# Performance work log

Measured on AMD Instinct MI355X. Metric: run time of the kernel, lower is better.

Reference implementation:

```python
import jax, jax.numpy as jnp
import numpy as np

D_MODEL = 768
CTX_DIM = 1024
N_HEAD = 12
N_QUERIES = 256
DIM_HEAD = D_MODEL // N_HEAD  # 64
INNER = DIM_HEAD * N_HEAD     # 768
EPS = 1e-5


def layernorm(x, w, b):
    mu = jnp.mean(x, axis=-1, keepdims=True)
    var = jnp.mean((x - mu) ** 2, axis=-1, keepdims=True)
    return (x - mu) * jax.lax.rsqrt(var + EPS) * w + b


def setup_inputs() -> dict:
    key = jax.random.key(0)
    ks = jax.random.split(key, 9)
    x = jax.random.normal(ks[0], (8, 4096, CTX_DIM), dtype=jnp.float32)
    query = jax.random.normal(ks[1], (N_QUERIES, D_MODEL), dtype=jnp.float32)
    # Linear weights stored [in, out] (y = x @ W)
    Wq = jax.random.normal(ks[2], (D_MODEL, INNER), dtype=jnp.float32) * 0.02
    Wkv = jax.random.normal(ks[3], (CTX_DIM, 2 * INNER), dtype=jnp.float32) * 0.02
    Wout = jax.random.normal(ks[4], (INNER, D_MODEL), dtype=jnp.float32) * 0.02
    ln_q_w = jnp.ones((D_MODEL,), jnp.float32)
    ln_q_b = jnp.zeros((D_MODEL,), jnp.float32)
    ln_k_w = jnp.ones((CTX_DIM,), jnp.float32)
    ln_k_b = jnp.zeros((CTX_DIM,), jnp.float32)
    return {"x": x, "query": query, "ln_q_w": ln_q_w, "ln_q_b": ln_q_b,
            "ln_k_w": ln_k_w, "ln_k_b": ln_k_b, "Wq": Wq, "Wkv": Wkv, "Wout": Wout}


def reference(x, query, ln_q_w, ln_q_b, ln_k_w, ln_k_b, Wq, Wkv, Wout):
    b = x.shape[0]
    h, dh = N_HEAD, DIM_HEAD
    scale = dh ** -0.5
    xk = x[:, None]  # b 1 n d  (m = 1)
    m, n = xk.shape[1], xk.shape[2]
    q = jnp.broadcast_to(query, (b, m) + query.shape)  # b m nq d
    xk = layernorm(xk, ln_k_w, ln_k_b)
    q = layernorm(q, ln_q_w, ln_q_b)
    q = q @ Wq                          # b m nq inner
    kv = xk @ Wkv                       # b m n 2*inner
    k, v = jnp.split(kv, 2, axis=-1)
    def split_heads(t):
        bb, tt, nn, _ = t.shape
        return t.reshape(bb, tt, nn, h, dh).transpose(0, 3, 1, 2, 4)  # b h t n dh
    q, k, v = split_heads(q), split_heads(k), split_heads(v)
    sim = jnp.einsum('bhtid,bhtjd->bhtij', q * scale, k)
    attn = jax.nn.softmax(sim, axis=-1)
    out = jnp.einsum('bhtij,bhtjd->bhtid', attn, v)  # b h t nq dh
    out = out.transpose(0, 2, 3, 1, 4).reshape(b, m, N_QUERIES, INNER)
    return (out @ Wout).squeeze(axis=1)  # b nq d_model
```

## Files before the change

### kernel.cpp

```cpp
#include <hip/hip_runtime.h>
#include <hip/hip_bf16.h>
#include <math.h>

#define B_    8
#define T_    4096
#define CD    1024
#define DM    768
#define NH    12
#define DH    64
#define NQ    256
#define INNER 768
#define NKV   1536
#define MKV   (B_*T_)
#define EPS   1e-5f
#define SCALE 0.125f

typedef __attribute__((ext_vector_type(8))) short short8;
typedef __attribute__((ext_vector_type(4))) float f32x4;

__device__ __forceinline__ unsigned short f2bf(float f) {
  union { __hip_bfloat16 h; unsigned short u; } cv;
  cv.h = __float2bfloat16(f);
  return cv.u;
}

__global__ __launch_bounds__(256) void tbw_kernel(
    const float* __restrict__ s0, unsigned short* __restrict__ d0,
    const float* __restrict__ s1, unsigned short* __restrict__ d1,
    const float* __restrict__ s2, unsigned short* __restrict__ d2) {
  int z = blockIdx.z;
  const float* src; unsigned short* dst; int SR, SC;
  if (z == 0)      { src = s0; dst = d0; SR = CD;    SC = NKV; }
  else if (z == 1) { src = s1; dst = d1; SR = DM;    SC = INNER; }
  else             { src = s2; dst = d2; SR = INNER; SC = DM; }
  int k0 = blockIdx.x * 32, n0 = blockIdx.y * 32;
  if (k0 >= SR || n0 >= SC) return;
  __shared__ float tile[32][33];
  int tid = threadIdx.x;
  int r = tid >> 3, c4 = (tid & 7) * 4;
  float4 v = *reinterpret_cast<const float4*>(&src[(size_t)(k0 + r) * SC + n0 + c4]);
  tile[r][c4 + 0] = v.x; tile[r][c4 + 1] = v.y; tile[r][c4 + 2] = v.z; tile[r][c4 + 3] = v.w;
  __syncthreads();
  ushort4 o4;
  o4.x = f2bf(tile[c4 + 0][r]);
  o4.y = f2bf(tile[c4 + 1][r]);
  o4.z = f2bf(tile[c4 + 2][r]);
  o4.w = f2bf(tile[c4 + 3][r]);
  *reinterpret_cast<ushort4*>(&dst[(size_t)(n0 + r) * SR + k0 + c4]) = o4;
}

__global__ __launch_bounds__(256) void qln_kernel(
    const float* __restrict__ query, const float* __restrict__ lnw,
    const float* __restrict__ lnb, unsigned short* __restrict__ qn) {
  int row = blockIdx.x, tid = threadIdx.x;
  __shared__ float rbuf[256];
  const float* qr = query + (size_t)row * DM;
  float v0 = qr[tid], v1 = qr[tid + 256], v2 = qr[tid + 512];
  rbuf[tid] = v0 + v1 + v2;
  __syncthreads();
  for (int o = 128; o > 0; o >>= 1) { if (tid < o) rbuf[tid] += rbuf[tid + o]; __syncthreads(); }
  float mean = rbuf[0] * (1.f / 768.f);
  __syncthreads();
  float d0 = v0 - mean, d1 = v1 - mean, d2 = v2 - mean;
  rbuf[tid] = d0 * d0 + d1 * d1 + d2 * d2;
  __syncthreads();
  for (int o = 128; o > 0; o >>= 1) { if (tid < o) rbuf[tid] += rbuf[tid + o]; __syncthreads(); }
  float var = rbuf[0] * (1.f / 768.f);
  float rs = rsqrtf(var + EPS);
  unsigned short* dst = qn + (size_t)row * DM;
  dst[tid]       = f2bf(d0 * rs * lnw[tid]       + lnb[tid]);
  dst[tid + 256] = f2bf(d1 * rs * lnw[tid + 256] + lnb[tid + 256]);
  dst[tid + 512] = f2bf(d2 * rs * lnw[tid + 512] + lnb[tid + 512]);
}

__global__ __launch_bounds__(256) void xnorm_kernel(
    const float* __restrict__ x, const float* __restrict__ lnw,
    const float* __restrict__ lnb, unsigned short* __restrict__ xn) {
  int row = blockIdx.x, tid = threadIdx.x;
  float4 v = reinterpret_cast<const float4*>(x + (size_t)row * CD)[tid];
  float s  = v.x + v.y + v.z + v.w;
  float ss = v.x * v.x + v.y * v.y + v.z * v.z + v.w * v.w;
  #pragma unroll
  for (int o = 32; o > 0; o >>= 1) { s += __shfl_down(s, o); ss += __shfl_down(ss, o); }
  __shared__ float sm[8];
  int wid = tid >> 6, lane = tid & 63;
  if (lane == 0) { sm[wid] = s; sm[4 + wid] = ss; }
  __syncthreads();
  float S  = sm[0] + sm[1] + sm[2] + sm[3];
  float SS = sm[4] + sm[5] + sm[6] + sm[7];
  float m  = S * (1.f / 1024.f);
  float var = SS * (1.f / 1024.f) - m * m;
  float rs = rsqrtf(fmaxf(var, 0.f) + EPS);
  float4 wv = reinterpret_cast<const float4*>(lnw)[tid];
  float4 bv = reinterpret_cast<const float4*>(lnb)[tid];
  ushort4 o4;
  o4.x = f2bf((v.x - m) * rs * wv.x + bv.x);
  o4.y = f2bf((v.y - m) * rs * wv.y + bv.y);
  o4.z = f2bf((v.z - m) * rs * wv.z + bv.z);
  o4.w = f2bf((v.w - m) * rs * wv.w + bv.w);
  reinterpret_cast<ushort4*>(xn + (size_t)row * CD)[tid] = o4;
}

template <int MODE>
__global__ __launch_bounds__(256) void gemm128_kernel(
    const unsigned short* __restrict__ A, const unsigned short* __restrict__ Bt,
    void* __restrict__ Cout, int N, int K, int nN, float scale, int swz) {
  __shared__ __attribute__((aligned(16))) unsigned short As[128 * 64];
  __shared__ __attribute__((aligned(16))) unsigned short Bs[128 * 64];
  int tid = threadIdx.x;
  int w = tid >> 6, lane = tid & 63;
  int bid = blockIdx.x;
  int sw = swz ? ((bid & 7) * ((int)gridDim.x >> 3) + (bid >> 3)) : bid;
  int mt = sw / nN, nt = sw % nN;
  int m0 = mt * 128, n0 = nt * 128;

  int srow[4], skoff[4];
  #pragma unroll
  for (int i = 0; i < 4; ++i) {
    int L = w * 4096 + i * 1024 + lane * 16;
    int row = L >> 7;
    int slot = (L >> 4) & 7;
    srow[i] = row;
    skoff[i] = ((slot ^ (row & 7)) << 3);
  }

  f32x4 acc[4][4];
  #pragma unroll
  for (int m = 0; m < 4; ++m)
    #pragma unroll
    for (int n = 0; n < 4; ++n) acc[m][n] = (f32x4){0.f, 0.f, 0.f, 0.f};

  int wr = w >> 1, wc = w & 1;
  int l15 = lane & 15, l4 = lane >> 4;

  for (int t = 0; t < K / 64; ++t) {
    int k0 = t * 64;
    #pragma unroll
    for (int i = 0; i < 4; ++i) {
      __builtin_amdgcn_global_load_lds(
          (const __attribute__((address_space(1))) void*)(A + (size_t)(m0 + srow[i]) * K + k0 + skoff[i]),
          (__attribute__((address_space(3))) void*)(As + w * 2048 + i * 512 + lane * 8),
          16, 0, 0);
    }
    #pragma unroll
    for (int i = 0; i < 4; ++i) {
      __builtin_amdgcn_global_load_lds(
          (const __attribute__((address_space(1))) void*)(Bt + (size_t)(n0 + srow[i]) * K + k0 + skoff[i]),
          (__attribute__((address_space(3))) void*)(Bs + w * 2048 + i * 512 + lane * 8),
          16, 0, 0);
    }
    __syncthreads();
    #pragma unroll
    for (int kh = 0; kh < 2; ++kh) {
      short8 af[4], bf[4];
      #pragma unroll
      for (int m = 0; m < 4; ++m) {
        int row = wr * 64 + m * 16 + l15;
        int byte = row * 128 + (((l4 + 4 * kh) ^ (row & 7)) << 4);
        af[m] = *reinterpret_cast<const short8*>(reinterpret_cast<const char*>(As) + byte);
      }
      #pragma unroll
      for (int n = 0; n < 4; ++n) {
        int row = wc * 64 + n * 16 + l15;
        int byte = row * 128 + (((l4 + 4 * kh) ^ (row & 7)) << 4);
        bf[n] = *reinterpret_cast<const short8*>(reinterpret_cast<const char*>(Bs) + byte);
      }
      #pragma unroll
      for (int m = 0; m < 4; ++m)
        #pragma unroll
        for (int n = 0; n < 4; ++n)
          acc[m][n] = __builtin_amdgcn_mfma_f32_16x16x32_bf16(af[m], bf[n], acc[m][n], 0, 0, 0);
    }
    __syncthreads();
  }

  #pragma unroll
  for (int m = 0; m < 4; ++m) {
    int grow = m0 + wr * 64 + m * 16 + l4 * 4;
    #pragma unroll
    for (int n = 0; n < 4; ++n) {
      int gcol = n0 + wc * 64 + n * 16 + l15;
      #pragma unroll
      for (int r = 0; r < 4; ++r) {
        if (MODE == 0)
          ((unsigned short*)Cout)[(size_t)(grow + r) * N + gcol] = f2bf(acc[m][n][r] * scale);
        else
          ((float*)Cout)[(size_t)(grow + r) * N + gcol] = acc[m][n][r];
      }
    }
  }
}

#define KBM 256
#define KBN 256
#define KBK 64
__global__ __launch_bounds__(512, 2) void kv_split_kernel(
    const unsigned short* __restrict__ xn, const unsigned short* __restrict__ wkvT,
    unsigned short* __restrict__ kvbK, unsigned short* __restrict__ vT) {
  __shared__ __attribute__((aligned(16))) unsigned short As[2][KBM * KBK];
  __shared__ __attribute__((aligned(16))) unsigned short Bs[2][KBN * KBK];
  int tid = threadIdx.x;
  int w = tid >> 6, lane = tid & 63;
  int wm = w >> 2, wn = w & 3;
  int l15 = lane & 15, l4 = lane >> 4;

  int bid = blockIdx.x;
  int sw = (bid & 7) * 96 + (bid >> 3);
  int mt = sw / (NKV / KBN), nt = sw % (NKV / KBN);
  int m0 = mt * KBM, n0 = nt * KBN;

  int srow[4], koff[4];
  #pragma unroll
  for (int i = 0; i < 4; ++i) {
    int r = i * 64 + (tid >> 3);
    srow[i] = r;
    koff[i] = (((tid & 7) ^ (r & 7)) << 3);
  }

  f32x4 acc[8][4];
  #pragma unroll
  for (int m = 0; m < 8; ++m)
    #pragma unroll
    for (int n = 0; n < 4; ++n) acc[m][n] = (f32x4){0.f, 0.f, 0.f, 0.f};

  #pragma unroll
  for (int i = 0; i < 4; ++i) {
    __builtin_amdgcn_global_load_lds(
        (const __attribute__((address_space(1))) void*)(xn + (size_t)(m0 + srow[i]) * CD + koff[i]),
        (__attribute__((address_space(3))) void*)(&As[0][0] + i * 4096 + tid * 8), 16, 0, 0);
    __builtin_amdgcn_global_load_lds(
        (const __attribute__((address_space(1))) void*)(wkvT + (size_t)(n0 + srow[i]) * CD + koff[i]),
        (__attribute__((address_space(3))) void*)(&Bs[0][0] + i * 4096 + tid * 8), 16, 0, 0);
  }
  __syncthreads();

  for (int t = 0; t < CD / KBK; ++t) {
    int cur = t & 1;
    if (t + 1 < CD / KBK) {
      int k0 = (t + 1) * KBK;
      #pragma unroll
      for (int i = 0; i < 4; ++i) {
        __builtin_amdgcn_global_load_lds(
            (const __attribute__((address_space(1))) void*)(xn + (size_t)(m0 + srow[i]) * CD + k0 + koff[i]),
            (__attribute__((address_space(3))) void*)(&As[cur ^ 1][0] + i * 4096 + tid * 8), 16, 0, 0);
        __builtin_amdgcn_global_load_lds(
            (const __attribute__((address_space(1))) void*)(wkvT + (size_t)(n0 + srow[i]) * CD + k0 + koff[i]),
            (__attribute__((address_space(3))) void*)(&Bs[cur ^ 1][0] + i * 4096 + tid * 8), 16, 0, 0);
      }
    }
    const char* Ab = reinterpret_cast<const char*>(&As[cur][0]);
    const char* Bb = reinterpret_cast<const char*>(&Bs[cur][0]);
    #pragma unroll
    for (int kh = 0; kh < 2; ++kh) {
      short8 bf[4];
      #pragma unroll
      for (int n = 0; n < 4; ++n) {
        int row = wn * 64 + n * 16 + l15;
        int byt = row * 128 + (((kh * 4 + l4) ^ (row & 7)) << 4);
        bf[n] = *reinterpret_cast<const short8*>(Bb + byt);
      }
      #pragma unroll
      for (int m = 0; m < 8; ++m) {
        int row = wm * 128 + m * 16 + l15;
        int byt = row * 128 + (((kh * 4 + l4) ^ (row & 7)) << 4);
        short8 af = *reinterpret_cast<const short8*>(Ab + byt);
        #pragma unroll
        for (int n = 0; n < 4; ++n)
          acc[m][n] = __builtin_amdgcn_mfma_f32_16x16x32_bf16(af, bf[n], acc[m][n], 0, 0, 0);
      }
    }
    __syncthreads();
  }

  if (nt < 3) {
    #pragma unroll
    for (int m = 0; m < 8; ++m) {
      int grow = m0 + wm * 128 + m * 16 + l4 * 4;
      #pragma unroll
      for (int n = 0; n < 4; ++n) {
        int gcol = nt * 256 + wn * 64 + n * 16 + l15;
        #pragma unroll
        for (int r = 0; r < 4; ++r)
          kvbK[(size_t)(grow + r) * INNER + gcol] = f2bf(acc[m][n][r]);
      }
    }
  } else {
    int b = m0 >> 12;
    int h = (nt - 3) * 4 + wn;
    #pragma unroll
    for (int m = 0; m < 8; ++m) {
      int j = (m0 & 4095) + wm * 128 + m * 16 + l4 * 4;
      #pragma unroll
      for (int n = 0; n < 4; ++n) {
        int d = n * 16 + l15;
        ushort4 o4;
        o4.x = f2bf(acc[m][n][0]); o4.y = f2bf(acc[m][n][1]);
        o4.z = f2bf(acc[m][n][2]); o4.w = f2bf(acc[m][n][3]);
        *reinterpret_cast<ushort4*>(&vT[((size_t)(b * NH + h) * DH + d) * T_ + j]) = o4;
      }
    }
  }
}

__global__ __launch_bounds__(256) void attn_mfma_kernel(
    const unsigned short* __restrict__ qpb, const unsigned short* __restrict__ kvbK,
    const unsigned short* __restrict__ vT,
    float* __restrict__ pO, float* __restrict__ pM, float* __restrict__ pL) {
  int bh = blockIdx.x, kc = blockIdx.y, qt = blockIdx.z;
  int b = bh / NH, h = bh % NH;
  __shared__ __attribute__((aligned(16))) unsigned short Ks[2][4096];
  __shared__ __attribute__((aligned(16))) unsigned short Vs[2][4096];
  __shared__ __attribute__((aligned(16))) unsigned short Ps[4][1024];
  int tid = threadIdx.x;
  int w = tid >> 6, lane = tid & 63;
  int l15 = lane & 15, l4 = lane >> 4;

  short8 qf[2];
  {
    const unsigned short* qb = qpb + (size_t)(qt * 64 + w * 16 + l15) * INNER + h * DH;
    qf[0] = *reinterpret_cast<const short8*>(qb + l4 * 8);
    qf[1] = *reinterpret_cast<const short8*>(qb + 32 + l4 * 8);
  }

  int srow0 = w * 16 + (lane >> 3);
  int srow1 = srow0 + 8;
  int koff0 = (((lane & 7) ^ (srow0 & 7)) << 3);
  int koff1 = (((lane & 7) ^ (srow1 & 7)) << 3);

  const size_t kbase = ((size_t)b * T_) * INNER + h * DH;
  const size_t vbase = ((size_t)bh * DH) * T_;

  auto stageKV = [&](int kt, int d) {
    int j0 = kc * 2048 + kt * 64;
    __builtin_amdgcn_global_load_lds(
        (const __attribute__((address_space(1))) void*)(kvbK + kbase + (size_t)(j0 + srow0) * INNER + koff0),
        (__attribute__((address_space(3))) void*)(&Ks[d][0] + w * 1024 + lane * 8), 16, 0, 0);
    __builtin_amdgcn_global_load_lds(
        (const __attribute__((address_space(1))) void*)(kvbK + kbase + (size_t)(j0 + srow1) * INNER + koff1),
        (__attribute__((address_space(3))) void*)(&Ks[d][0] + w * 1024 + 512 + lane * 8), 16, 0, 0);
    __builtin_amdgcn_global_load_lds(
        (const __attribute__((address_space(1))) void*)(vT + vbase + (size_t)srow0 * T_ + j0 + koff0),
        (__attribute__((address_space(3))) void*)(&Vs[d][0] + w * 1024 + lane * 8), 16, 0, 0);
    __builtin_amdgcn_global_load_lds(
        (const __attribute__((address_space(1))) void*)(vT + vbase + (size_t)srow1 * T_ + j0 + koff1),
        (__attribute__((address_space(3))) void*)(&Vs[d][0] + w * 1024 + 512 + lane * 8), 16, 0, 0);
  };

  f32x4 o[4];
  #pragma unroll
  for (int i = 0; i < 4; ++i) o[i] = (f32x4){0.f, 0.f, 0.f, 0.f};
  float m_run = -1e30f, l_run = 0.f;

  stageKV(0, 0);

  for (int kt = 0; kt < 32; ++kt) {
    int cur = kt & 1;
    if (kt + 1 < 32) {
      stageKV(kt + 1, cur ^ 1);
      asm volatile("s_waitcnt vmcnt(4)" ::: "memory");
    } else {
      asm volatile("s_waitcnt vmcnt(0)" ::: "memory");
    }
    __builtin_amdgcn_s_barrier();
    __builtin_amdgcn_sched_barrier(0);

    const char* Kb = reinterpret_cast<const char*>(&Ks[cur][0]);
    const char* Vb = reinterpret_cast<const char*>(&Vs[cur][0]);

    f32x4 st[4];
    __builtin_amdgcn_s_setprio(1);
    #pragma unroll
    for (int sub = 0; sub < 4; ++sub) {
      st[sub] = (f32x4){0.f, 0.f, 0.f, 0.f};
      #pragma unroll
      for (int hf = 0; hf < 2; ++hf) {
        int row = sub * 16 + l15;
        int byt = row * 128 + (((l4 + 4 * hf) ^ (row & 7)) << 4);
        short8 kf = *reinterpret_cast<const short8*>(Kb + byt);
        st[sub] = __builtin_amdgcn_mfma_f32_16x16x32_bf16(kf, qf[hf], st[sub], 0, 0, 0);
      }
    }
    __builtin_amdgcn_s_setprio(0);

    float tmax = -1e30f;
    #pragma unroll
    for (int sub = 0; sub < 4; ++sub)
      #pragma unroll
      for (int r = 0; r < 4; ++r) tmax = fmaxf(tmax, st[sub][r]);
    tmax = fmaxf(tmax, __shfl_xor(tmax, 16));
    tmax = fmaxf(tmax, __shfl_xor(tmax, 32));

    if (__ballot(tmax > m_run + 8.f)) {
      float m_new = fmaxf(m_run, tmax);
      float alpha = __expf(m_run - m_new);
      float ao[4];
      #pragma unroll
      for (int r = 0; r < 4; ++r) ao[r] = __shfl(alpha, (l4 << 2) | r);
      #pragma unroll
      for (int ds = 0; ds < 4; ++ds)
        #pragma unroll
        for (int r = 0; r < 4; ++r) o[ds][r] *= ao[r];
      l_run *= alpha;
      m_run = m_new;
    }

    float psum = 0.f;
    #pragma unroll
    for (int sub = 0; sub < 4; ++sub) {
      float p0 = __expf(st[sub][0] - m_run);
      float p1 = __expf(st[sub][1] - m_run);
      float p2 = __expf(st[sub][2] - m_run);
      float p3 = __expf(st[sub][3] - m_run);
      psum += (p0 + p1) + (p2 + p3);
      unsigned int u0 = (unsigned int)f2bf(p0) | ((unsigned int)f2bf(p1) << 16);
      unsigned int u1 = (unsigned int)f2bf(p2) | ((unsigned int)f2bf(p3) << 16);
      int slot = (sub * 2 + (l4 >> 1)) ^ (l15 & 7);
      int byt = l15 * 128 + (slot << 4) + (l4 & 1) * 8;
      uint2 uv; uv.x = u0; uv.y = u1;
      *reinterpret_cast<uint2*>(reinterpret_cast<char*>(Ps[w]) + byt) = uv;
    }
    psum += __shfl_xor(psum, 16);
    psum += __shfl_xor(psum, 32);
    l_run += psum;

    short8 pa[2];
    #pragma unroll
    for (int hf = 0; hf < 2; ++hf) {
      int byt = l15 * 128 + ((((hf << 2) + l4) ^ (l15 & 7)) << 4);
      pa[hf] = *reinterpret_cast<const short8*>(reinterpret_cast<const char*>(Ps[w]) + byt);
    }
    __builtin_amdgcn_s_setprio(1);
    #pragma unroll
    for (int ds = 0; ds < 4; ++ds) {
      #pragma unroll
      for (int hf = 0; hf < 2; ++hf) {
        int row = ds * 16 + l15;
        int byt = row * 128 + (((l4 + 4 * hf) ^ (row & 7)) << 4);
        short8 vf = *reinterpret_cast<const short8*>(Vb + byt);
        o[ds] = __builtin_amdgcn_mfma_f32_16x16x32_bf16(pa[hf], vf, o[ds], 0, 0, 0);
      }
    }
    __builtin_amdgcn_s_setprio(0);
    __builtin_amdgcn_s_barrier();
    __builtin_amdgcn_sched_barrier(0);
  }

  int pidx = bh * 2 + kc;
  int qrow0 = qt * 64 + w * 16;
  if (l4 == 0) {
    pM[(size_t)pidx * NQ + qrow0 + l15] = m_run;
    pL[(size_t)pidx * NQ + qrow0 + l15] = l_run;
  }
  #pragma unroll
  for (int ds = 0; ds < 4; ++ds)
    #pragma unroll
    for (int r = 0; r < 4; ++r)
      pO[((size_t)pidx * NQ + qrow0 + l4 * 4 + r) * DH + ds * 16 + l15] = o[ds][r];
}

__global__ __launch_bounds__(256) void attn_combine_kernel(
    const float* __restrict__ pO, const float* __restrict__ pM,
    const float* __restrict__ pL, unsigned short* __restrict__ attn_out) {
  int qt = blockIdx.x, bh = blockIdx.y;
  int b = bh / NH, h = bh % NH;
  int tid = threadIdx.x;
  #pragma unroll
  for (int e = 0; e < 16; ++e) {
    int idx = e * 256 + tid;
    int r = idx >> 6, d = idx & 63;
    int row = qt * 64 + r;
    size_t i0 = (size_t)(bh * 2 + 0) * NQ + row;
    size_t i1 = (size_t)(bh * 2 + 1) * NQ + row;
    float m1 = pM[i0], m2 = pM[i1], l1 = pL[i0], l2 = pL[i1];
    float M = fmaxf(m1, m2);
    float w1 = __expf(m1 - M), w2 = __expf(m2 - M);
    float L = l1 * w1 + l2 * w2;
    float oo = (pO[i0 * DH + d] * w1 + pO[i1 * DH + d] * w2) / L;
    attn_out[((size_t)b * NQ + row) * INNER + h * DH + d] = f2bf(oo);
  }
}

extern "C" void kernel_launch(void* const* d_in, const int* in_sizes, int n_in,
                              void* d_out, int out_size, void* d_ws, size_t ws_size,
                              hipStream_t stream) {
  const float* x      = (const float*)d_in[0];
  const float* query  = (const float*)d_in[1];
  const float* ln_q_w = (const float*)d_in[2];
  const float* ln_q_b = (const float*)d_in[3];
  const float* ln_k_w = (const float*)d_in[4];
  const float* ln_k_b = (const float*)d_in[5];
  const float* Wq     = (const float*)d_in[6];
  const float* Wkv    = (const float*)d_in[7];
  const float* Wout   = (const float*)d_in[8];
  float* out = (float*)d_out;

  unsigned short* qpb   = (unsigned short*)d_ws;
  unsigned short* xn    = qpb + (size_t)NQ * INNER;
  unsigned short* wkvT  = xn + (size_t)MKV * CD;
  unsigned short* kvbK  = wkvT + (size_t)NKV * CD;
  unsigned short* vT    = kvbK + (size_t)MKV * INNER;
  float* pO    = (float*)(vT + (size_t)MKV * INNER);
  float* pM    = pO + (size_t)B_ * NH * 2 * NQ * DH;
  float* pL    = pM + (size_t)B_ * NH * 2 * NQ;
  unsigned short* attnb = (unsigned short*)(pL + (size_t)B_ * NH * 2 * NQ);
  unsigned short* qn    = attnb + (size_t)B_ * NQ * INNER;
  unsigned short* WqT   = qn + (size_t)NQ * DM;
  unsigned short* WoutT = WqT + (size_t)DM * INNER;

  hipLaunchKernelGGL(tbw_kernel, dim3(CD / 32, NKV / 32, 3), dim3(256), 0, stream,
                     Wkv, wkvT, Wq, WqT, Wout, WoutT);
  hipLaunchKernelGGL(qln_kernel, dim3(NQ), dim3(256), 0, stream,
                     query, ln_q_w, ln_q_b, qn);
  hipLaunchKernelGGL((gemm128_kernel<0>), dim3((NQ / 128) * (INNER / 128)), dim3(256), 0, stream,
                     qn, WqT, (void*)qpb, INNER, DM, INNER / 128, SCALE, 0);
  hipLaunchKernelGGL(xnorm_kernel, dim3(MKV), dim3(256), 0, stream,
                     x, ln_k_w, ln_k_b, xn);
  hipLaunchKernelGGL(kv_split_kernel, dim3((MKV / KBM) * (NKV / KBN)), dim3(512), 0, stream,
                     xn, wkvT, kvbK, vT);
  hipLaunchKernelGGL(attn_mfma_kernel, dim3(B_ * NH, 2, 4), dim3(256), 0, stream,
                     qpb, kvbK, vT, pO, pM, pL);
  hipLaunchKernelGGL(attn_combine_kernel, dim3(4, B_ * NH), dim3(256), 0, stream,
                     pO, pM, pL, attnb);
  hipLaunchKernelGGL((gemm128_kernel<1>), dim3((B_ * NQ / 128) * (DM / 128)), dim3(256), 0, stream,
                     attnb, WoutT, (void*)out, DM, INNER, DM / 128, 1.f, 1);
}
```

Baseline: 263.4 us.

## Fuse split-KV attention combine into output projection GEMM

Removes the separate combine kernel and the bf16 attention-output buffer. The output GEMM now builds its A tile directly from the two partial attention results (pO/pM/pL), rescaling and normalising them per head-chunk before writing to LDS. This saves one launch and a global round trip of the combined activations. In exchange, each N-tile block recomputes the combine, redundantly across 6 column tiles, and the A-tile load is no longer an async global-to-LDS copy.

```diff
diff --git a/kernel.cpp b/kernel.cpp
--- a/kernel.cpp
+++ b/kernel.cpp
@@ -458,25 +458,113 @@
       pO[((size_t)pidx * NQ + qrow0 + l4 * 4 + r) * DH + ds * 16 + l15] = o[ds][r];
 }
 
-__global__ __launch_bounds__(256) void attn_combine_kernel(
+__global__ __launch_bounds__(256) void outfuse_kernel(
     const float* __restrict__ pO, const float* __restrict__ pM,
-    const float* __restrict__ pL, unsigned short* __restrict__ attn_out) {
-  int qt = blockIdx.x, bh = blockIdx.y;
-  int b = bh / NH, h = bh % NH;
+    const float* __restrict__ pL, const unsigned short* __restrict__ WoutT,
+    float* __restrict__ out) {
+  __shared__ __attribute__((aligned(16))) unsigned short As[128 * 64];
+  __shared__ __attribute__((aligned(16))) unsigned short Bs[128 * 64];
   int tid = threadIdx.x;
-  #pragma unroll
-  for (int e = 0; e < 16; ++e) {
-    int idx = e * 256 + tid;
-    int r = idx >> 6, d = idx & 63;
-    int row = qt * 64 + r;
-    size_t i0 = (size_t)(bh * 2 + 0) * NQ + row;
-    size_t i1 = (size_t)(bh * 2 + 1) * NQ + row;
-    float m1 = pM[i0], m2 = pM[i1], l1 = pL[i0], l2 = pL[i1];
-    float M = fmaxf(m1, m2);
-    float w1 = __expf(m1 - M), w2 = __expf(m2 - M);
-    float L = l1 * w1 + l2 * w2;
-    float oo = (pO[i0 * DH + d] * w1 + pO[i1 * DH + d] * w2) / L;
-    attn_out[((size_t)b * NQ + row) * INNER + h * DH + d] = f2bf(oo);
+  int w = tid >> 6, lane = tid & 63;
+  int bid = blockIdx.x;
+  int sw = (bid & 7) * 12 + (bid >> 3);
+  int mt = sw / 6, nt = sw % 6;
+  int m0 = mt * 128, n0 = nt * 128;
+
+  int srow[4], skoff[4];
+  #pragma unroll
+  for (int i = 0; i < 4; ++i) {
+    int L = w * 4096 + i * 1024 + lane * 16;
+    int row = L >> 7;
+    int slot = (L >> 4) & 7;
+    srow[i] = row;
+    skoff[i] = ((slot ^ (row & 7)) << 3);
+  }
+
+  f32x4 acc[4][4];
+  #pragma unroll
+  for (int m = 0; m < 4; ++m)
+    #pragma unroll
+    for (int n = 0; n < 4; ++n) acc[m][n] = (f32x4){0.f, 0.f, 0.f, 0.f};
+
+  int wr = w >> 1, wc = w & 1;
+  int l15 = lane & 15, l4 = lane >> 4;
+
+  for (int t = 0; t < NH; ++t) {
+    #pragma unroll
+    for (int i = 0; i < 4; ++i) {
+      int lin = i * 256 + tid;
+      int r = lin >> 3, sl = lin & 7;
+      int gr = m0 + r;
+      int b = gr >> 8, q = gr & 255;
+      size_t i0 = ((size_t)(b * NH + t) * 2) * NQ + q;
+      size_t i1 = i0 + NQ;
+      float m1 = pM[i0], m2 = pM[i1], l1 = pL[i0], l2 = pL[i1];
+      float Mx = fmaxf(m1, m2);
+      float w1 = __expf(m1 - Mx), w2 = __expf(m2 - Mx);
+      float invL = 1.f / (l1 * w1 + l2 * w2);
+      w1 *= invL; w2 *= invL;
+      const float* p0 = pO + i0 * DH + sl * 8;
+      const float* p1 = pO + i1 * DH + sl * 8;
+      float4 a0 = *reinterpret_cast<const float4*>(p0);
+      float4 a1 = *reinterpret_cast<const float4*>(p0 + 4);
+      float4 b0 = *reinterpret_cast<const float4*>(p1);
+      float4 b1 = *reinterpret_cast<const float4*>(p1 + 4);
+      short8 v8;
+      v8[0] = (short)f2bf(a0.x * w1 + b0.x * w2);
+      v8[1] = (short)f2bf(a0.y * w1 + b0.y * w2);
+      v8[2] = (short)f2bf(a0.z * w1 + b0.z * w2);
+      v8[3] = (short)f2bf(a0.w * w1 + b0.w * w2);
+      v8[4] = (short)f2bf(a1.x * w1 + b1.x * w2);
+      v8[5] = (short)f2bf(a1.y * w1 + b1.y * w2);
+      v8[6] = (short)f2bf(a1.z * w1 + b1.z * w2);
+      v8[7] = (short)f2bf(a1.w * w1 + b1.w * w2);
+      *reinterpret_cast<short8*>(reinterpret_cast<char*>(As) +
+                                 r * 128 + ((sl ^ (r & 7)) << 4)) = v8;
+    }
+    int k0 = t * 64;
+    #pragma unroll
+    for (int i = 0; i < 4; ++i) {
+      __builtin_amdgcn_global_load_lds(
+          (const __attribute__((address_space(1))) void*)(WoutT + (size_t)(n0 + srow[i]) * INNER + k0 + skoff[i]),
+          (__attribute__((address_space(3))) void*)(Bs + w * 2048 + i * 512 + lane * 8),
+          16, 0, 0);
+    }
+    __syncthreads();
+    #pragma unroll
+    for (int kh = 0; kh < 2; ++kh) {
+      short8 af[4], bf[4];
+      #pragma unroll
+      for (int m = 0; m < 4; ++m) {
+        int row = wr * 64 + m * 16 + l15;
+        int byte = row * 128 + (((l4 + 4 * kh) ^ (row & 7)) << 4);
+        af[m] = *reinterpret_cast<const short8*>(reinterpret_cast<const char*>(As) + byte);
+      }
+      #pragma unroll
+      for (int n = 0; n < 4; ++n) {
+        int row = wc * 64 + n * 16 + l15;
+        int byte = row * 128 + (((l4 + 4 * kh) ^ (row & 7)) << 4);
+        bf[n] = *reinterpret_cast<const short8*>(reinterpret_cast<const char*>(Bs) + byte);
+      }
+      #pragma unroll
+      for (int m = 0; m < 4; ++m)
+        #pragma unroll
+        for (int n = 0; n < 4; ++n)
+          acc[m][n] = __builtin_amdgcn_mfma_f32_16x16x32_bf16(af[m], bf[n], acc[m][n], 0, 0, 0);
+    }
+    __syncthreads();
+  }
+
+  #pragma unroll
+  for (int m = 0; m < 4; ++m) {
+    int grow = m0 + wr * 64 + m * 16 + l4 * 4;
+    #pragma unroll
+    for (int n = 0; n < 4; ++n) {
+      int gcol = n0 + wc * 64 + n * 16 + l15;
+      #pragma unroll
+      for (int r = 0; r < 4; ++r)
+        out[(size_t)(grow + r) * DM + gcol] = acc[m][n][r];
+    }
   }
 }
 
@@ -502,8 +590,7 @@
   float* pO    = (float*)(vT + (size_t)MKV * INNER);
   float* pM    = pO + (size_t)B_ * NH * 2 * NQ * DH;
   float* pL    = pM + (size_t)B_ * NH * 2 * NQ;
-  unsigned short* attnb = (unsigned short*)(pL + (size_t)B_ * NH * 2 * NQ);
-  unsigned short* qn    = attnb + (size_t)B_ * NQ * INNER;
+  unsigned short* qn    = (unsigned short*)(pL + (size_t)B_ * NH * 2 * NQ);
   unsigned short* WqT   = qn + (size_t)NQ * DM;
   unsigned short* WoutT = WqT + (size_t)DM * INNER;
 
@@ -519,8 +606,6 @@
                      xn, wkvT, kvbK, vT);
   hipLaunchKernelGGL(attn_mfma_kernel, dim3(B_ * NH, 2, 4), dim3(256), 0, stream,
                      qpb, kvbK, vT, pO, pM, pL);
-  hipLaunchKernelGGL(attn_combine_kernel, dim3(4, B_ * NH), dim3(256), 0, stream,
-                     pO, pM, pL, attnb);
-  hipLaunchKernelGGL((gemm128_kernel<1>), dim3((B_ * NQ / 128) * (DM / 128)), dim3(256), 0, stream,
-                     attnb, WoutT, (void*)out, DM, INNER, DM / 128, 1.f, 1);
-}
+  hipLaunchKernelGGL(outfuse_kernel, dim3((B_ * NQ / 128) * (DM / 128)), dim3(256), 0, stream,
+                     pO, pM, pL, WoutT, out);
+}
```

Result: no change. 263.4 us (+0.0%).
